# Optimization experiments

Measured on AMD Instinct MI355X. Metric: run time of the kernel, lower is better.

Reference implementation:

```python
import jax, jax.numpy as jnp
import numpy as np

NB, B, L, D, H = 4, 4, 1024, 512, 8
E = D // H  # head dim = 64
SCALE = 1.0 / np.sqrt(E)


def setup_inputs() -> dict:
    key = jax.random.key(0)
    ks = jax.random.split(key, 18)
    w = lambda k, shape: (jax.random.normal(k, shape, dtype=jnp.float32) * 0.02)
    inp = {
        'x': jax.random.normal(ks[0], (NB, B, L, D), dtype=jnp.float32),
        # per-block intra-attention projections, stored [in, out] (x @ W + b)
        'Wq': w(ks[1], (NB, D, D)), 'bq': w(ks[2], (NB, D)),
        'Wk': w(ks[3], (NB, D, D)), 'bk': w(ks[4], (NB, D)),
        'Wv': w(ks[5], (NB, D, D)), 'bv': w(ks[6], (NB, D)),
        'Wo': w(ks[7], (NB, D, D)), 'bo': w(ks[8], (NB, D)),
        # shared inter (router) attention projections
        'iWq': w(ks[9], (D, D)), 'ibq': w(ks[10], (D,)),
        'iWk': w(ks[11], (D, D)), 'ibk': w(ks[12], (D,)),
        'iWv': w(ks[13], (D, D)), 'ibv': w(ks[14], (D,)),
        'iWo': w(ks[15], (D, D)), 'ibo': w(ks[16], (D,)),
    }
    return inp


def _full_attn(q, k, v):
    # q,k,v: [..., S, H, E] with batch dims leading; unmasked FullAttention
    scores = jnp.einsum('...lhe,...she->...hls', q, k) * SCALE
    A = jax.nn.softmax(scores, axis=-1)
    return jnp.einsum('...hls,...shd->...lhd', A, v)


def reference(x, Wq, bq, Wk, bk, Wv, bv, Wo, bo,
              iWq, ibq, iWk, ibk, iWv, ibv, iWo, ibo):
    # ---- intra attention, vectorized over the NB blocks ----
    proj = lambda W, b: (jnp.einsum('nbld,nde->nble', x, W) + b[:, None, None, :])
    q = proj(Wq, bq).reshape(NB, B, L, H, E)
    k = proj(Wk, bk).reshape(NB, B, L, H, E)
    v = proj(Wv, bv).reshape(NB, B, L, H, E)
    o = _full_attn(q, k, v).reshape(NB, B, L, D)
    x_intra = jnp.einsum('nbld,nde->nble', o, Wo) + bo[:, None, None, :]

    # ---- inter attention over router tokens (last token of each block) ----
    routers = jnp.transpose(x_intra[:, :, -1, :], (1, 0, 2))  # [B, NB, D]
    rq = (routers @ iWq + ibq).reshape(B, NB, H, E)
    rk = (routers @ iWk + ibk).reshape(B, NB, H, E)
    rv = (routers @ iWv + ibv).reshape(B, NB, H, E)
    ro = _full_attn(rq, rk, rv).reshape(B, NB, D)
    x_inter = ro @ iWo + ibo  # [B, NB, D]

    # replace each block's last (router) token with its inter-attended version
    x_out = x_intra.at[:, :, -1, :].set(jnp.transpose(x_inter, (1, 0, 2)))
    return x_out  # [NB, B, L, D]
```

## Files before the change

kernel.cpp:

```cpp
#include <hip/hip_runtime.h>
#include <math.h>

#define NBV 4
#define BBV 4
#define LLV 1024
#define DDV 512
#define HHV 8
#define EEV 64

typedef unsigned short u16;
typedef _Float16 half8 __attribute__((ext_vector_type(8)));
typedef float f32x4 __attribute__((ext_vector_type(4)));

#define QSCALE 0.1803368801111243f

__device__ __forceinline__ u16 f2h(float f) {
  union { _Float16 h; u16 u; } v; v.h = (_Float16)f; return v.u;
}
__device__ __forceinline__ unsigned pkrtz(float a, float b) {
  typedef __fp16 fp16x2 __attribute__((ext_vector_type(2)));
  union { fp16x2 h; unsigned u; } c;
  c.h = __builtin_amdgcn_cvt_pkrtz(a, b);
  return c.u;
}
__device__ __forceinline__ void gload16(const void* g, void* l) {
  __builtin_amdgcn_global_load_lds(
      (const __attribute__((address_space(1))) unsigned int*)g,
      (__attribute__((address_space(3))) unsigned int*)l, 16, 0, 0);
}

__global__ __launch_bounds__(256) void convert(
    const float* __restrict__ x,
    const float* __restrict__ Wq, const float* __restrict__ Wk,
    const float* __restrict__ Wv, const float* __restrict__ Wo,
    u16* __restrict__ x_t, u16* __restrict__ wt, u16* __restrict__ wo)
{
  const int bid = blockIdx.x;
  if (bid < 4096) {
    const int t = bid * 256 + threadIdx.x;
    const int lane = t & 63;
    const int f = (t >> 6) & 7;
    const int kt = (t >> 9) & 15;
    const int rt = t >> 13;
    const int r = rt * 128 + f * 16 + (lane & 15);
    const int k0 = kt * 32 + (lane >> 4) * 8;
    const float* s = x + (size_t)r * 512 + k0;
    float4 v0 = *(const float4*)s;
    float4 v1 = *(const float4*)(s + 4);
    float vv[8] = {v0.x, v0.y, v0.z, v0.w, v1.x, v1.y, v1.z, v1.w};
    union { u16 s16[8]; uint4 v; } H;
#pragma unroll
    for (int j = 0; j < 8; ++j) H.s16[j] = f2h(vv[j]);
    *(uint4*)(x_t + (size_t)t * 8) = H.v;
  } else {
    const int qkv = (bid < 5632);
    const int t = (qkv ? (bid - 4096) : (bid - 5632)) * 256 + threadIdx.x;
    const int z = t >> 15;
    const int tl = t & 32767;
    const int lane = tl & 63;
    const int f = (tl >> 6) & 7;
    const int kt = (tl >> 9) & 15;
    const int rt = tl >> 13;
    const float* W;
    u16* dst;
    if (qkv) {
      const int nb = z / 3, p = z - nb * 3;
      W = (p == 0 ? Wq : p == 1 ? Wk : Wv) + (size_t)nb * 262144;
      dst = wt;
    } else {
      W = Wo + (size_t)z * 262144;
      dst = wo;
    }
    const int r = rt * 128 + f * 16 + (lane & 15);
    const int k0 = kt * 32 + (lane >> 4) * 8;
    union { u16 s16[8]; uint4 v; } H;
#pragma unroll
    for (int j = 0; j < 8; ++j) H.s16[j] = f2h(W[(size_t)(k0 + j) * 512 + r]);
    *(uint4*)(dst + (size_t)z * 262144 + (size_t)tl * 8) = H.v;
  }
}

template <int MODE>
__global__ __launch_bounds__(256) void gemm_f16(
    const u16* __restrict__ Aw, const u16* __restrict__ Bx,
    const float* __restrict__ bias0, const float* __restrict__ bias1,
    const float* __restrict__ bias2,
    u16* __restrict__ q_b, u16* __restrict__ k_b, u16* __restrict__ v_t,
    float* __restrict__ Cout)
{
  __shared__ __align__(16) u16 SM[24576];
  u16* As = SM;
  u16* Bs = SM + 12288;

  const int tid = threadIdx.x;
  const int lane = tid & 63, w = tid >> 6;
  const int l15 = lane & 15, l4 = lane >> 4;
  const int bid = blockIdx.x;

  int mt, nt, z;
  if (MODE == 0) {
    const int wgid = (bid & 7) * 192 + (bid >> 3);
    mt = wgid & 3; nt = (wgid >> 2) & 31; z = wgid >> 7;
  } else {
    const int wgid = (bid & 7) * 64 + (bid >> 3);
    mt = wgid & 31; nt = (wgid >> 5) & 3; z = wgid >> 7;
  }

  int nb, p;
  const u16 *A, *B;
  if (MODE == 0) {
    nb = z / 3; p = z - nb * 3;
    A = Aw + (size_t)z * 262144;
    B = Bx + (size_t)nb * 2097152;
  } else {
    nb = z; p = 0;
    A = Aw + (size_t)z * 2097152;
    B = Bx + (size_t)z * 262144;
  }

  const f32x4 z4 = {0.f, 0.f, 0.f, 0.f};
  f32x4 acc[4][4];
#pragma unroll
  for (int i = 0; i < 4; ++i)
#pragma unroll
    for (int j = 0; j < 4; ++j) acc[i][j] = z4;

#define GSTAGE(buf, kt)                                                        \
  {                                                                            \
    const u16* ap = A + ((size_t)((mt * 16 + (kt)) * 8) + w * 2) * 512 + lane * 8; \
    const u16* bp = B + ((size_t)((nt * 16 + (kt)) * 8) + w * 2) * 512 + lane * 8; \
    gload16(ap,       As + (buf) * 4096 + (w * 2 + 0) * 512);                  \
    gload16(ap + 512, As + (buf) * 4096 + (w * 2 + 1) * 512);                  \
    gload16(bp,       Bs + (buf) * 4096 + (w * 2 + 0) * 512);                  \
    gload16(bp + 512, Bs + (buf) * 4096 + (w * 2 + 1) * 512);                  \
  }

  GSTAGE(0, 0);
  GSTAGE(1, 1);
  GSTAGE(2, 2);
  asm volatile("s_waitcnt vmcnt(8)" ::: "memory");
  __builtin_amdgcn_sched_barrier(0);
  __builtin_amdgcn_s_barrier();
  __builtin_amdgcn_sched_barrier(0);

  for (int kt = 0; kt < 16; ++kt) {
    const int cur = kt % 3;

    half8 a[4], b[4];
#pragma unroll
    for (int m = 0; m < 4; ++m)
      a[m] = *(const half8*)(As + cur * 4096 + ((w >> 1) * 4 + m) * 512 + lane * 8);
#pragma unroll
    for (int n = 0; n < 4; ++n)
      b[n] = *(const half8*)(Bs + cur * 4096 + ((w & 1) * 4 + n) * 512 + lane * 8);
    __builtin_amdgcn_s_setprio(1);
#pragma unroll
    for (int m = 0; m < 4; ++m)
#pragma unroll
      for (int n = 0; n < 4; ++n)
        acc[m][n] = __builtin_amdgcn_mfma_f32_16x16x32_f16(a[m], b[n], acc[m][n], 0, 0, 0);
    __builtin_amdgcn_s_setprio(0);

    asm volatile("s_waitcnt lgkmcnt(0)" ::: "memory");
    if (kt <= 13) { asm volatile("s_waitcnt vmcnt(4)" ::: "memory"); }
    else          { asm volatile("s_waitcnt vmcnt(0)" ::: "memory"); }
    __builtin_amdgcn_sched_barrier(0);
    __builtin_amdgcn_s_barrier();
    __builtin_amdgcn_sched_barrier(0);
    if (kt < 13) GSTAGE(cur, kt + 3);
  }
#undef GSTAGE

  if (MODE == 0) {
    const float* bias = (p == 0 ? bias0 : p == 1 ? bias1 : bias2) + nb * 512;
    const int hh = w >> 1;
    __syncthreads();
    if (p < 2) {
      const float scl = (p == 0) ? QSCALE : 1.0f;
#pragma unroll
      for (int mm = 0; mm < 4; ++mm) {
        const int c = mm * 4 + l4;
#pragma unroll
        for (int nn = 0; nn < 4; ++nn) {
          const int tok = (w & 1) * 64 + nn * 16 + l15;
          ushort4 pk;
#pragma unroll
          for (int i = 0; i < 4; ++i) {
            const int mf = mt * 128 + hh * 64 + mm * 16 + l4 * 4 + i;
            ((u16*)&pk)[i] = f2h((acc[mm][nn][i] + bias[mf]) * scl);
          }
          *(ushort4*)((char*)SM + hh * 17408 + tok * 136 +
                      ((c ^ (tok & 15)) * 8)) = pk;
        }
      }
      __syncthreads();
      u16* dst = (p == 0 ? q_b : k_b);
#pragma unroll
      for (int i = 0; i < 16; ++i) {
        const int idx = i * 256 + tid;
        const int h2 = idx >> 11, tok = (idx >> 4) & 127, c = idx & 15;
        ushort4 v = *(const ushort4*)((char*)SM + h2 * 17408 + tok * 136 +
                                      ((c ^ (tok & 15)) * 8));
        const int ltok = nt * 128 + tok;
        const int headf = (nb * 4 + (ltok >> 10)) * 8 + mt * 2 + h2;
        *(ushort4*)(dst + (size_t)headf * 65536 + (ltok & 1023) * 64 + c * 4) = v;
      }
    } else {
#pragma unroll
      for (int mm = 0; mm < 4; ++mm) {
#pragma unroll
        for (int nn = 0; nn < 4; ++nn) {
          const int tok = (w & 1) * 64 + nn * 16 + l15;
#pragma unroll
          for (int r = 0; r < 4; ++r) {
            const int e = mm * 16 + l4 * 4 + r;
            const int mf = mt * 128 + hh * 64 + e;
            *(u16*)((char*)SM + hh * 17408 + e * 264 + tok * 2) =
                f2h(acc[mm][nn][r] + bias[mf]);
          }
        }
      }
      __syncthreads();
#pragma unroll
      for (int i = 0; i < 16; ++i) {
        const int idx = i * 256 + tid;
        const int h2 = idx >> 11, rem = idx & 2047;
        const int e = rem >> 5, s = rem & 31;
        uint2 v = *(const uint2*)((char*)SM + h2 * 17408 + e * 264 + s * 8);
        const int headf = (nb * 4 + (nt >> 3)) * 8 + mt * 2 + h2;
        *(uint2*)(v_t + (size_t)headf * 65536 + e * 1024 +
                  (nt & 7) * 128 + s * 4) = v;
      }
    }
  } else {
#pragma unroll
    for (int mm = 0; mm < 4; ++mm) {
#pragma unroll
      for (int nn = 0; nn < 4; ++nn) {
        const int m0 = mt * 128 + ((w >> 1) * 4 + mm) * 16 + l4 * 4;
        const int n  = nt * 128 + ((w & 1) * 4 + nn) * 16 + l15;
        const float bz = bias0[nb * 512 + n];
#pragma unroll
        for (int r = 0; r < 4; ++r)
          Cout[((size_t)nb * 4096 + m0 + r) * 512 + n] = acc[mm][nn][r] + bz;
      }
    }
  }
}

__global__ __launch_bounds__(512, 4) void attn_mfma(
    const u16* __restrict__ Qb, const u16* __restrict__ Kb,
    const u16* __restrict__ Vt, u16* __restrict__ o_t)
{
  __shared__ __align__(16) u16 SM[34816];
  u16* KL = SM;
  u16* VL = SM + 12288;
  u16* PL = SM + 24576;

  const int tid = threadIdx.x;
  const int lane = tid & 63, w = tid >> 6;
  const int l15 = lane & 15, l4 = lane >> 4;
  const int sb = blockIdx.x;
  const int head = sb & 127;
  const int qt = sb >> 7;
  const size_t hbase = (size_t)head * 65536;
  const int q0 = qt * 256;

  const f32x4 z4 = {0.f, 0.f, 0.f, 0.f};
  const _Float16 one_h = (_Float16)1.0f;
  const half8 ones = {one_h, one_h, one_h, one_h, one_h, one_h, one_h, one_h};
  f32x4 oacc[2][4], ls[2];
#pragma unroll
  for (int qm = 0; qm < 2; ++qm) {
    ls[qm] = z4;
#pragma unroll
    for (int ef = 0; ef < 4; ++ef) oacc[qm][ef] = z4;
  }

  const int rowl = lane >> 3;
  const int colx = ((lane & 7) ^ rowl) * 8;

#define STAGE(buf, kt0)                                                        \
  {                                                                            \
    gload16(Kb + hbase + (size_t)((kt0) + w * 8 + rowl) * 64 + colx,           \
            KL + (buf) * 4096 + w * 512);                                      \
    gload16(Vt + hbase + (size_t)(w * 8 + rowl) * 1024 + (kt0) + colx,         \
            VL + (buf) * 4096 + w * 512);                                      \
  }

  half8 qf[2][2];
#pragma unroll
  for (int qm = 0; qm < 2; ++qm) {
    const u16* qp = Qb + hbase + (size_t)(q0 + w * 32 + qm * 16 + l15) * 64 + l4 * 8;
    qf[qm][0] = *(const half8*)qp;
    qf[qm][1] = *(const half8*)(qp + 32);
  }
  __builtin_amdgcn_sched_barrier(0);

  STAGE(0, 0);
  STAGE(1, 64);
  STAGE(2, 128);
  asm volatile("s_waitcnt vmcnt(4)" ::: "memory");
  __builtin_amdgcn_sched_barrier(0);
  __builtin_amdgcn_s_barrier();
  __builtin_amdgcn_sched_barrier(0);

  char* Pw = (char*)(PL + w * 1280);

  for (int t = 0; t < 16; ++t) {
    const int cur = t % 3;

    f32x4 st[2][4];
#pragma unroll
    for (int qm = 0; qm < 2; ++qm)
#pragma unroll
      for (int kf = 0; kf < 4; ++kf) st[qm][kf] = z4;

    __builtin_amdgcn_s_setprio(1);
#pragma unroll
    for (int kf = 0; kf < 4; ++kf) {
      const int key = kf * 16 + l15;
      const int swz = (key & 7) << 4;
#pragma unroll
      for (int eh = 0; eh < 2; ++eh) {
        half8 af = *(const half8*)((char*)(KL + cur * 4096) +
                     ((key * 128 + eh * 64 + l4 * 16) ^ swz));
        st[0][kf] = __builtin_amdgcn_mfma_f32_16x16x32_f16(af, qf[0][eh], st[0][kf], 0, 0, 0);
        st[1][kf] = __builtin_amdgcn_mfma_f32_16x16x32_f16(af, qf[1][eh], st[1][kf], 0, 0, 0);
      }
    }
    __builtin_amdgcn_s_setprio(0);

#pragma unroll
    for (int kh = 0; kh < 2; ++kh) {
#pragma unroll
      for (int qm = 0; qm < 2; ++qm) {
        const int row = qm * 16 + l15;
#pragma unroll
        for (int kf2 = 0; kf2 < 2; ++kf2) {
          const int kf = kh * 2 + kf2;
          float e0 = __builtin_amdgcn_exp2f(st[qm][kf][0]);
          float e1 = __builtin_amdgcn_exp2f(st[qm][kf][1]);
          float e2 = __builtin_amdgcn_exp2f(st[qm][kf][2]);
          float e3 = __builtin_amdgcn_exp2f(st[qm][kf][3]);
          uint2 d;
          d.x = pkrtz(e0, e1);
          d.y = pkrtz(e2, e3);
          *(uint2*)(Pw + row * 80 + kf2 * 32 + l4 * 8) = d;
        }
      }
      __builtin_amdgcn_s_setprio(1);
      half8 pa0 = *(const half8*)(Pw + l15 * 80 + l4 * 16);
      half8 pa1 = *(const half8*)(Pw + (16 + l15) * 80 + l4 * 16);
      ls[0] = __builtin_amdgcn_mfma_f32_16x16x32_f16(pa0, ones, ls[0], 0, 0, 0);
      ls[1] = __builtin_amdgcn_mfma_f32_16x16x32_f16(pa1, ones, ls[1], 0, 0, 0);
#pragma unroll
      for (int ef = 0; ef < 4; ++ef) {
        const int e = ef * 16 + l15;
        half8 vb2 = *(const half8*)((char*)(VL + cur * 4096) +
                      ((e * 128 + kh * 64 + l4 * 16) ^ ((e & 7) << 4)));
        oacc[0][ef] = __builtin_amdgcn_mfma_f32_16x16x32_f16(pa0, vb2, oacc[0][ef], 0, 0, 0);
        oacc[1][ef] = __builtin_amdgcn_mfma_f32_16x16x32_f16(pa1, vb2, oacc[1][ef], 0, 0, 0);
      }
      __builtin_amdgcn_s_setprio(0);
    }

    asm volatile("s_waitcnt lgkmcnt(0)" ::: "memory");
    if (t <= 13) { asm volatile("s_waitcnt vmcnt(2)" ::: "memory"); }
    else         { asm volatile("s_waitcnt vmcnt(0)" ::: "memory"); }
    __builtin_amdgcn_sched_barrier(0);
    __builtin_amdgcn_s_barrier();
    __builtin_amdgcn_sched_barrier(0);
    if (t < 13) STAGE(cur, (t + 3) * 64);
  }
#undef STAGE

  char* Ot = (char*)SM;
#pragma unroll
  for (int qm = 0; qm < 2; ++qm) {
    f32x4 iv;
#pragma unroll
    for (int r = 0; r < 4; ++r) iv[r] = 1.0f / ls[qm][r];
#pragma unroll
    for (int ef = 0; ef < 4; ++ef)
#pragma unroll
      for (int r = 0; r < 4; ++r) {
        const int tokl = w * 32 + qm * 16 + l4 * 4 + r;
        const int dl = ef * 16 + l15;
        *(u16*)(Ot + ((tokl * 128 + dl * 2) ^ ((tokl & 7) << 4))) =
            f2h(oacc[qm][ef][r] * iv[r]);
      }
  }
  __syncthreads();

  const int nb = head >> 5, bb = (head >> 3) & 3, h = head & 7;
  u16* abase = o_t + (size_t)nb * 2097152;
#pragma unroll
  for (int i = 0; i < 4; ++i) {
    const int gidx = i * 512 + tid;
    const int rt_loc = gidx >> 10;
    const int rem = gidx & 1023;
    const int kh = rem >> 9, f = (rem >> 6) & 7, ln = rem & 63;
    const int tokl = rt_loc * 128 + f * 16 + (ln & 15);
    const int dl = kh * 32 + (ln >> 4) * 8;
    uint4 vvv = *(const uint4*)(Ot + ((tokl * 128 + dl * 2) ^ ((tokl & 7) << 4)));
    const int rt = bb * 8 + qt * 2 + rt_loc;
    *(uint4*)(abase + ((size_t)((rt * 16 + h * 2 + kh) * 8 + f) * 512 + ln * 8)) = vvv;
  }
}

__global__ __launch_bounds__(256) void inter_qa(
    const float* __restrict__ xout,
    const float* __restrict__ iWq, const float* __restrict__ iWk,
    const float* __restrict__ iWv,
    const float* __restrict__ ibq, const float* __restrict__ ibk,
    const float* __restrict__ ibv,
    float* __restrict__ ro)
{
    __shared__ float Rs[4][512];
    __shared__ float Pp[12][16][68];
    __shared__ float R2[3][4][64];
    const int tid = threadIdx.x;
    const int b = blockIdx.x >> 3, h = blockIdx.x & 7;

    for (int t = tid; t < 512; t += 256) {
        const int n = t >> 7, k4 = (t & 127) * 4;
        *(float4*)&Rs[n][k4] =
            *(const float4*)&xout[(((size_t)(n * BBV + b) * LLV) + (LLV - 1)) * DDV + k4];
    }
    __syncthreads();

    const int kq = tid >> 4;
    const int c4 = (tid & 15) * 4;
    const int col = h * 64 + c4;

    f32x4 acc[3][4];
#pragma unroll
    for (int p = 0; p < 3; ++p)
#pragma unroll
        for (int n = 0; n < 4; ++n) acc[p][n] = (f32x4){0.f, 0.f, 0.f, 0.f};

    for (int i = 0; i < 32; ++i) {
        const int k = i * 16 + kq;
        const float4 wq = *(const float4*)&iWq[(size_t)k * 512 + col];
        const float4 wk = *(const float4*)&iWk[(size_t)k * 512 + col];
        const float4 wv = *(const float4*)&iWv[(size_t)k * 512 + col];
#pragma unroll
        for (int n = 0; n < 4; ++n) {
            const float rv_ = Rs[n][k];
            acc[0][n][0] += rv_ * wq.x; acc[0][n][1] += rv_ * wq.y;
            acc[0][n][2] += rv_ * wq.z; acc[0][n][3] += rv_ * wq.w;
            acc[1][n][0] += rv_ * wk.x; acc[1][n][1] += rv_ * wk.y;
            acc[1][n][2] += rv_ * wk.z; acc[1][n][3] += rv_ * wk.w;
            acc[2][n][0] += rv_ * wv.x; acc[2][n][1] += rv_ * wv.y;
            acc[2][n][2] += rv_ * wv.z; acc[2][n][3] += rv_ * wv.w;
        }
    }
#pragma unroll
    for (int p = 0; p < 3; ++p)
#pragma unroll
        for (int n = 0; n < 4; ++n)
            *(f32x4*)&Pp[p * 4 + n][kq][c4] = acc[p][n];
    __syncthreads();

    for (int t = tid; t < 768; t += 256) {
        const int row = t >> 6, e = t & 63;
        float s = 0.f;
#pragma unroll
        for (int q = 0; q < 16; ++q) s += Pp[row][q][e];
        const int p = row >> 2, n = row & 3;
        const float* bias = (p == 0 ? ibq : p == 1 ? ibk : ibv);
        R2[p][n][e] = s + bias[h * 64 + e];
    }
    __syncthreads();

    if (tid < 64) {
        float qv[4], kv[4], vv[4];
#pragma unroll
        for (int n = 0; n < 4; ++n) {
            qv[n] = R2[0][n][tid]; kv[n] = R2[1][n][tid]; vv[n] = R2[2][n][tid];
        }
        float s[4][4];
#pragma unroll
        for (int n = 0; n < 4; ++n)
#pragma unroll
            for (int m = 0; m < 4; ++m) {
                float prod = qv[n] * kv[m];
#pragma unroll
                for (int off = 1; off < 64; off <<= 1) prod += __shfl_xor(prod, off);
                s[n][m] = prod * 0.125f;
            }
#pragma unroll
        for (int n = 0; n < 4; ++n) {
            float mx = fmaxf(fmaxf(s[n][0], s[n][1]), fmaxf(s[n][2], s[n][3]));
            float pr[4], den = 0.f, ov = 0.f;
#pragma unroll
            for (int m = 0; m < 4; ++m) { pr[m] = __expf(s[n][m] - mx); den += pr[m]; }
#pragma unroll
            for (int m = 0; m < 4; ++m) ov += pr[m] * vv[m];
            ro[(size_t)(b * 4 + n) * 512 + h * 64 + tid] = ov / den;
        }
    }
}

__global__ __launch_bounds__(256) void inter_out(
    const float* __restrict__ ro, const float* __restrict__ iWo,
    const float* __restrict__ ibo, float* __restrict__ out)
{
    __shared__ float Rs[16][512];
    __shared__ float P[16][68];
    const int tid = threadIdx.x;
    for (int t = tid; t < 2048; t += 256)
        *(float4*)&Rs[t >> 7][(t & 127) * 4] = *(const float4*)&ro[t * 4];
    __syncthreads();

    const int cb = blockIdx.x * 64;
    const int c4 = (tid & 15) * 4;
    const int kq = tid >> 4;

    f32x4 acc[16];
#pragma unroll
    for (int r = 0; r < 16; ++r) acc[r] = (f32x4){0.f, 0.f, 0.f, 0.f};

    for (int i = 0; i < 32; ++i) {
        const int k = i * 16 + kq;
        const float4 wv = *(const float4*)&iWo[(size_t)k * 512 + cb + c4];
#pragma unroll
        for (int r = 0; r < 16; ++r) {
            const float rv_ = Rs[r][k];
            acc[r][0] += rv_ * wv.x;
            acc[r][1] += rv_ * wv.y;
            acc[r][2] += rv_ * wv.z;
            acc[r][3] += rv_ * wv.w;
        }
    }

#pragma unroll
    for (int r = 0; r < 16; ++r) {
        *(f32x4*)&P[kq][c4] = acc[r];
        __syncthreads();
        if (tid < 64) {
            float s = 0.f;
#pragma unroll
            for (int q = 0; q < 16; ++q) s += P[q][tid];
            const int b = r >> 2, n = r & 3;
            out[(((size_t)(n * BBV + b) * LLV) + (LLV - 1)) * DDV + cb + tid] =
                s + ibo[cb + tid];
        }
        __syncthreads();
    }
}

extern "C" void kernel_launch(void* const* d_in, const int* in_sizes, int n_in,
                              void* d_out, int out_size, void* d_ws, size_t ws_size,
                              hipStream_t stream)
{
    (void)in_sizes; (void)n_in; (void)out_size; (void)ws_size;
    const float* x   = (const float*)d_in[0];
    const float* Wq  = (const float*)d_in[1];  const float* bq  = (const float*)d_in[2];
    const float* Wk  = (const float*)d_in[3];  const float* bk  = (const float*)d_in[4];
    const float* Wv  = (const float*)d_in[5];  const float* bv  = (const float*)d_in[6];
    const float* Wo  = (const float*)d_in[7];  const float* bo  = (const float*)d_in[8];
    const float* iWq = (const float*)d_in[9];  const float* ibq = (const float*)d_in[10];
    const float* iWk = (const float*)d_in[11]; const float* ibk = (const float*)d_in[12];
    const float* iWv = (const float*)d_in[13]; const float* ibv = (const float*)d_in[14];
    const float* iWo = (const float*)d_in[15]; const float* ibo = (const float*)d_in[16];
    float* out = (float*)d_out;

    char* W = (char*)d_ws;
    u16* x_t  = (u16*)(W);
    u16* wt   = (u16*)(W + 16777216);
    u16* wo   = (u16*)(W + 33554432);
    u16* q_b  = (u16*)(W + 35651584);
    u16* k_b  = (u16*)(W + 52428800);
    u16* v_t  = (u16*)(W + 69206016);
    u16* o_t  = (u16*)(W + 85983232);
    float* ro = (float*)(W + 102760448);

    convert<<<6144, 256, 0, stream>>>(x, Wq, Wk, Wv, Wo, x_t, wt, wo);
    gemm_f16<0><<<1536, 256, 0, stream>>>(
        wt, x_t, bq, bk, bv, q_b, k_b, v_t, nullptr);
    attn_mfma<<<512, 512, 0, stream>>>(q_b, k_b, v_t, o_t);
    gemm_f16<1><<<512, 256, 0, stream>>>(
        o_t, wo, bo, nullptr, nullptr, nullptr, nullptr, nullptr, out);
    inter_qa<<<32, 256, 0, stream>>>(out, iWq, iWk, iWv, ibq, ibk, ibv, ro);
    inter_out<<<8, 256, 0, stream>>>(ro, iWo, ibo, out);
}
```

Before: 140.1 us.

## Software-pipeline QK^T one tile ahead of softmax and PV in attention loop

```diff
diff --git a/kernel.cpp b/kernel.cpp
--- a/kernel.cpp
+++ b/kernel.cpp
@@ -288,6 +288,24 @@
             VL + (buf) * 4096 + w * 512);                                      \
   }
 
+#define QKT(dst, bufbase)                                                      \
+  {                                                                            \
+    __builtin_amdgcn_s_setprio(1);                                             \
+    _Pragma("unroll")                                                          \
+    for (int kf = 0; kf < 4; ++kf) {                                           \
+      const int key = kf * 16 + l15;                                           \
+      const int swz = (key & 7) << 4;                                          \
+      _Pragma("unroll")                                                        \
+      for (int eh = 0; eh < 2; ++eh) {                                         \
+        half8 af = *(const half8*)((char*)(bufbase) +                          \
+                     ((key * 128 + eh * 64 + l4 * 16) ^ swz));                 \
+        dst[0][kf] = __builtin_amdgcn_mfma_f32_16x16x32_f16(af, qf[0][eh], dst[0][kf], 0, 0, 0); \
+        dst[1][kf] = __builtin_amdgcn_mfma_f32_16x16x32_f16(af, qf[1][eh], dst[1][kf], 0, 0, 0); \
+      }                                                                        \
+    }                                                                          \
+    __builtin_amdgcn_s_setprio(0);                                             \
+  }
+
   half8 qf[2][2];
 #pragma unroll
   for (int qm = 0; qm < 2; ++qm) {
@@ -300,36 +318,29 @@
   STAGE(0, 0);
   STAGE(1, 64);
   STAGE(2, 128);
-  asm volatile("s_waitcnt vmcnt(4)" ::: "memory");
+  asm volatile("s_waitcnt vmcnt(2)" ::: "memory");
   __builtin_amdgcn_sched_barrier(0);
   __builtin_amdgcn_s_barrier();
   __builtin_amdgcn_sched_barrier(0);
 
   char* Pw = (char*)(PL + w * 1280);
 
+  f32x4 stc[2][4];
+#pragma unroll
+  for (int qm = 0; qm < 2; ++qm)
+#pragma unroll
+    for (int kf = 0; kf < 4; ++kf) stc[qm][kf] = z4;
+  QKT(stc, KL);
+
   for (int t = 0; t < 16; ++t) {
     const int cur = t % 3;
 
-    f32x4 st[2][4];
+    f32x4 stn[2][4];
 #pragma unroll
     for (int qm = 0; qm < 2; ++qm)
 #pragma unroll
-      for (int kf = 0; kf < 4; ++kf) st[qm][kf] = z4;
-
-    __builtin_amdgcn_s_setprio(1);
-#pragma unroll
-    for (int kf = 0; kf < 4; ++kf) {
-      const int key = kf * 16 + l15;
-      const int swz = (key & 7) << 4;
-#pragma unroll
-      for (int eh = 0; eh < 2; ++eh) {
-        half8 af = *(const half8*)((char*)(KL + cur * 4096) +
-                     ((key * 128 + eh * 64 + l4 * 16) ^ swz));
-        st[0][kf] = __builtin_amdgcn_mfma_f32_16x16x32_f16(af, qf[0][eh], st[0][kf], 0, 0, 0);
-        st[1][kf] = __builtin_amdgcn_mfma_f32_16x16x32_f16(af, qf[1][eh], st[1][kf], 0, 0, 0);
-      }
-    }
-    __builtin_amdgcn_s_setprio(0);
+      for (int kf = 0; kf < 4; ++kf) stn[qm][kf] = z4;
+    if (t < 15) QKT(stn, KL + ((t + 1) % 3) * 4096);
 
 #pragma unroll
     for (int kh = 0; kh < 2; ++kh) {
@@ -339,10 +350,10 @@
 #pragma unroll
         for (int kf2 = 0; kf2 < 2; ++kf2) {
           const int kf = kh * 2 + kf2;
-          float e0 = __builtin_amdgcn_exp2f(st[qm][kf][0]);
-          float e1 = __builtin_amdgcn_exp2f(st[qm][kf][1]);
-          float e2 = __builtin_amdgcn_exp2f(st[qm][kf][2]);
-          float e3 = __builtin_amdgcn_exp2f(st[qm][kf][3]);
+          float e0 = __builtin_amdgcn_exp2f(stc[qm][kf][0]);
+          float e1 = __builtin_amdgcn_exp2f(stc[qm][kf][1]);
+          float e2 = __builtin_amdgcn_exp2f(stc[qm][kf][2]);
+          float e3 = __builtin_amdgcn_exp2f(stc[qm][kf][3]);
           uint2 d;
           d.x = pkrtz(e0, e1);
           d.y = pkrtz(e2, e3);
@@ -365,15 +376,22 @@
       __builtin_amdgcn_s_setprio(0);
     }
 
+    if (t < 15) {
+#pragma unroll
+      for (int qm = 0; qm < 2; ++qm)
+#pragma unroll
+        for (int kf = 0; kf < 4; ++kf) stc[qm][kf] = stn[qm][kf];
+    }
+
     asm volatile("s_waitcnt lgkmcnt(0)" ::: "memory");
-    if (t <= 13) { asm volatile("s_waitcnt vmcnt(2)" ::: "memory"); }
-    else         { asm volatile("s_waitcnt vmcnt(0)" ::: "memory"); }
+    asm volatile("s_waitcnt vmcnt(0)" ::: "memory");
     __builtin_amdgcn_sched_barrier(0);
     __builtin_amdgcn_s_barrier();
     __builtin_amdgcn_sched_barrier(0);
     if (t < 13) STAGE(cur, (t + 3) * 64);
   }
 #undef STAGE
+#undef QKT
 
   char* Ot = (char*)SM;
 #pragma unroll
```

New measurement: 227.6 us. 62.4% more time.
